# Optimization experiments

Hardware: AMD Instinct MI355X
Metric: run time of the kernel (lower is better)

## Reference

```python
import jax, jax.numpy as jnp
import numpy as np

D = 1024
H = 16
HD = D // H
MLP = 4 * D


def _lin(key, fin, fout):
    k1, k2 = jax.random.split(key)
    lim = 1.0 / np.sqrt(fin)
    W = jax.random.uniform(k1, (fin, fout), minval=-lim, maxval=lim, dtype=jnp.float32)
    b = jax.random.uniform(k2, (fout,), minval=-lim, maxval=lim, dtype=jnp.float32)
    return W, b


def setup_inputs() -> dict:
    key = jax.random.key(0)
    ks = jax.random.split(key, 10)
    x = jax.random.normal(ks[0], (4, 2048, D), dtype=jnp.float32)
    time_emb = jax.random.normal(ks[1], (4, D), dtype=jnp.float32)
    Wqkv, bqkv = _lin(ks[2], D, 3 * D)
    Wproj, bproj = _lin(ks[3], D, D)
    W1, b1 = _lin(ks[4], D, MLP)
    W2, b2 = _lin(ks[5], MLP, D)
    Wt, bt = _lin(ks[6], D, 6 * D)
    g1 = jnp.ones((D,), jnp.float32); be1 = jnp.zeros((D,), jnp.float32)
    g2 = jnp.ones((D,), jnp.float32); be2 = jnp.zeros((D,), jnp.float32)
    return {"x": x, "time_emb": time_emb, "Wqkv": Wqkv, "bqkv": bqkv,
            "Wproj": Wproj, "bproj": bproj, "W1": W1, "b1": b1, "W2": W2, "b2": b2,
            "Wt": Wt, "bt": bt, "g1": g1, "be1": be1, "g2": g2, "be2": be2}


def layernorm(x, g, b, eps=1e-5):
    mu = jnp.mean(x, axis=-1, keepdims=True)
    var = jnp.var(x, axis=-1, keepdims=True)
    return (x - mu) * jax.lax.rsqrt(var + eps) * g + b


def attention(h, Wqkv, bqkv, Wproj, bproj):
    B, L, _ = h.shape
    qkv = (h @ Wqkv + bqkv).reshape(B, L, 3, H, HD)
    q, k, v = jnp.moveaxis(qkv, 2, 0)  # each [B,L,H,HD]
    scale = HD ** -0.5
    attn = jnp.einsum('blhd,bmhd->bhlm', q, k) * scale
    attn = jax.nn.softmax(attn, axis=-1)
    out = jnp.einsum('bhlm,bmhd->blhd', attn, v).reshape(B, L, D)
    return out @ Wproj + bproj


def reference(x, time_emb, Wqkv, bqkv, Wproj, bproj, W1, b1, W2, b2, Wt, bt, g1, be1, g2, be2):
    tp = (jax.nn.silu(time_emb) @ Wt + bt)[:, None, :]  # [B,1,6D]
    shift_msa, scale_msa, gate_msa, shift_mlp, scale_mlp, gate_mlp = jnp.split(tp, 6, axis=-1)
    h = layernorm(x, g1, be1)
    h = h * (1.0 + scale_msa) + shift_msa
    h = attention(h, Wqkv, bqkv, Wproj, bproj)
    x = x + gate_msa * h
    h = layernorm(x, g2, be2)
    h = h * (1.0 + scale_mlp) + shift_mlp
    h = jax.nn.gelu(h @ W1 + b1, approximate=False) @ W2 + b2
    x = x + gate_mlp * h
    return x
```

## Files before the change

### kernel.cpp

```cpp
#include <hip/hip_runtime.h>
#include <hip/hip_bf16.h>
#include <math.h>


typedef __attribute__((ext_vector_type(8))) __bf16 bf16x8;
typedef __attribute__((ext_vector_type(4))) float f32x4;

union FragU { uint4 u; bf16x8 b; };

#define AS1(p) ((const __attribute__((address_space(1))) void*)(p))
#define AS3(p) ((__attribute__((address_space(3))) void*)(p))

__device__ __forceinline__ float bflo(uint u) {
    union { uint i; float f; } v; v.i = u << 16; return v.f;
}
__device__ __forceinline__ float bfhi(uint u) {
    union { uint i; float f; } v; v.i = u & 0xffff0000u; return v.f;
}
__device__ __forceinline__ ushort f2bf(float f) {
    union { float f; uint i; } v; v.f = f;
    uint r = (v.i + 0x7fffu + ((v.i >> 16) & 1u)) >> 16;
    return (ushort)r;
}
__device__ __forceinline__ uint pkbf(float a, float b) {
    return __builtin_amdgcn_perm(__float_as_uint(b), __float_as_uint(a), 0x07060302u);
}
__device__ __forceinline__ void stval(ushort* p, float v) { *p = f2bf(v); }
__device__ __forceinline__ void stval(float* p, float v) { *p = v; }

__device__ __forceinline__ float gelu_f(float x) {
    float y = 0.7978845608f * (x + 0.044715f * x * x * x);
    float e = exp2f(y * 2.88539008178f);
    float t = 1.f - 2.f / (1.f + e);
    return 0.5f * x * (1.f + t);
}

__global__ __launch_bounds__(256) void transpose_f2b(const float* __restrict__ in,
                                                     ushort* __restrict__ out,
                                                     int R, int C) {
    __shared__ ushort t[32][33];
    int c0 = blockIdx.x * 32, r0 = blockIdx.y * 32;
    int tx = threadIdx.x, ty = threadIdx.y;
#pragma unroll
    for (int i = 0; i < 32; i += 8)
        t[ty + i][tx] = f2bf(in[(size_t)(r0 + ty + i) * C + c0 + tx]);
    __syncthreads();
#pragma unroll
    for (int i = 0; i < 32; i += 8)
        out[(size_t)(c0 + ty + i) * R + r0 + tx] = t[tx][ty + i];
}

__global__ __launch_bounds__(256) void transpose_v(const ushort* __restrict__ qkv,
                                                   ushort* __restrict__ vT) {
    int bh = blockIdx.x >> 5, lt = blockIdx.x & 31;
    int b = bh >> 4, h = bh & 15;
    int d = threadIdx.x & 63, lg = threadIdx.x >> 6;
    const ushort* src = qkv + (size_t)b * 2048 * 3072 + 2048 + h * 64 + d;
#pragma unroll
    for (int g = 0; g < 2; g++) {
        int l0 = lt * 64 + lg * 16 + g * 8;
        ushort v[8];
#pragma unroll
        for (int i = 0; i < 8; i++) v[i] = src[(size_t)(l0 + i) * 3072];
        *(uint4*)&vT[((size_t)bh * 64 + d) * 2048 + l0] = *(uint4*)v;
    }
}

__global__ __launch_bounds__(256) void tp_gemm(const float* __restrict__ te,
                                               const ushort* __restrict__ WtT,
                                               const float* __restrict__ bt,
                                               float* __restrict__ tp) {
    int w = blockIdx.x * 4 + (threadIdx.x >> 6);
    int lane = threadIdx.x & 63;
    int b = w / 6144, n = w % 6144;
    const ushort* wr = WtT + (size_t)n * 1024;
    const float* tr = te + (size_t)b * 1024;
    float s = 0.f;
#pragma unroll
    for (int i = 0; i < 16; i++) {
        int k = lane + 64 * i;
        float t = tr[k];
        float sil = t / (1.f + __expf(-t));
        s += sil * bflo((uint)wr[k]);
    }
#pragma unroll
    for (int x = 32; x; x >>= 1) s += __shfl_xor(s, x);
    if (lane == 0) tp[(size_t)b * 6144 + n] = s + bt[n];
}

__global__ __launch_bounds__(256) void ln_mod(const float* __restrict__ x,
                                              const float* __restrict__ tpb,
                                              const float* __restrict__ g,
                                              const float* __restrict__ be,
                                              ushort* __restrict__ out,
                                              int shift_off, int scale_off) {
    __shared__ float2 sred[4];
    int row = blockIdx.x;
    int b = row >> 11;
    int tid = threadIdx.x;
    float4 f = *(const float4*)&x[(size_t)row * 1024 + tid * 4];
    float v[4] = {f.x, f.y, f.z, f.w};
    float s = v[0] + v[1] + v[2] + v[3];
    float s2 = v[0] * v[0] + v[1] * v[1] + v[2] * v[2] + v[3] * v[3];
#pragma unroll
    for (int m = 32; m; m >>= 1) { s += __shfl_xor(s, m); s2 += __shfl_xor(s2, m); }
    if ((tid & 63) == 0) sred[tid >> 6] = make_float2(s, s2);
    __syncthreads();
    s = sred[0].x + sred[1].x + sred[2].x + sred[3].x;
    s2 = sred[0].y + sred[1].y + sred[2].y + sred[3].y;
    float mu = s * (1.f / 1024.f);
    float var = s2 * (1.f / 1024.f) - mu * mu;
    float rs = rsqrtf(var + 1e-5f);
    const float* tprow = tpb + (size_t)b * 6144;
    ushort o4[4];
#pragma unroll
    for (int t = 0; t < 4; t++) {
        int c = tid * 4 + t;
        float y = (v[t] - mu) * rs * g[c] + be[c];
        y = y * (1.f + tprow[scale_off + c]) + tprow[shift_off + c];
        o4[t] = f2bf(y);
    }
    *(uint2*)&out[(size_t)row * 1024 + tid * 4] = *(uint2*)o4;
}

template <int EPI, typename OT>
__global__ __launch_bounds__(256) void gemm_bt(const ushort* __restrict__ A,
                                               const ushort* __restrict__ BT,
                                               const float* __restrict__ bias,
                                               OT* __restrict__ C,
                                               int M, int N, int K,
                                               const float* __restrict__ res,
                                               const float* __restrict__ tpb,
                                               int goff) {
    __shared__ __align__(16) ushort As[2][128 * 32];
    __shared__ __align__(16) ushort Bs[2][128 * 32];
    int m0 = blockIdx.y * 128, n0 = blockIdx.x * 128;
    int tid = threadIdx.x;
    int wid = tid >> 6, lane = tid & 63;
    int wy = wid >> 1, wx = wid & 1;
    int r16 = lane & 15;
    int q8 = (lane >> 4) << 3;

    f32x4 acc[4][4];
#pragma unroll
    for (int i = 0; i < 4; i++)
#pragma unroll
        for (int j = 0; j < 4; j++) acc[i][j] = (f32x4){0.f, 0.f, 0.f, 0.f};

    int sr = tid >> 2;
    int sc = (tid & 3) << 3;
    const ushort* Abase = A + (size_t)(m0 + sr) * K + sc;
    const ushort* Bbase = BT + (size_t)(n0 + sr) * K + sc;

    for (int k0 = 0; k0 < K; k0 += 64) {
#pragma unroll
        for (int c = 0; c < 2; c++) {
            ushort* AsW = As[c] + wid * 512;
            ushort* BsW = Bs[c] + wid * 512;
            int kk = k0 + 32 * c;
            __builtin_amdgcn_global_load_lds(AS1(Abase + kk), AS3(AsW), 16, 0, 0);
            __builtin_amdgcn_global_load_lds(AS1(Abase + (size_t)64 * K + kk), AS3(AsW + 2048), 16, 0, 0);
            __builtin_amdgcn_global_load_lds(AS1(Bbase + kk), AS3(BsW), 16, 0, 0);
            __builtin_amdgcn_global_load_lds(AS1(Bbase + (size_t)64 * K + kk), AS3(BsW + 2048), 16, 0, 0);
        }
        __syncthreads();
#pragma unroll
        for (int c = 0; c < 2; c++) {
            FragU fa[4], fb[4];
#pragma unroll
            for (int i = 0; i < 4; i++)
                fa[i].u = *(const uint4*)&As[c][(wy * 64 + i * 16 + r16) * 32 + q8];
#pragma unroll
            for (int j = 0; j < 4; j++)
                fb[j].u = *(const uint4*)&Bs[c][(wx * 64 + j * 16 + r16) * 32 + q8];
#pragma unroll
            for (int i = 0; i < 4; i++)
#pragma unroll
                for (int j = 0; j < 4; j++)
                    acc[i][j] = __builtin_amdgcn_mfma_f32_16x16x32_bf16(fa[i].b, fb[j].b, acc[i][j], 0, 0, 0);
        }
        __syncthreads();
    }

    int q4 = (lane >> 4) << 2;
#pragma unroll
    for (int i = 0; i < 4; i++) {
#pragma unroll
        for (int j = 0; j < 4; j++) {
            int col = n0 + wx * 64 + j * 16 + r16;
            float bv = bias[col];
#pragma unroll
            for (int t = 0; t < 4; t++) {
                int row = m0 + wy * 64 + i * 16 + q4 + t;
                float v = acc[i][j][t] + bv;
                if constexpr (EPI == 1) {
                    v = gelu_f(v);
                }
                if constexpr (EPI == 2) {
                    float rv = res[(size_t)row * N + col];
                    float gate = tpb[(size_t)(row >> 11) * 6144 + goff + col];
                    v = rv + gate * v;
                }
                stval(&C[(size_t)row * N + col], v);
            }
        }
    }
}

__global__ __launch_bounds__(256, 5) void attn_mfma(const ushort* __restrict__ qkv,
                                                    const ushort* __restrict__ vT,
                                                    ushort* __restrict__ out) {
    __shared__ __align__(16) ushort Ks[64 * 72];
    __shared__ __align__(16) ushort Vs[64 * 72];
    __shared__ __align__(16) ushort Ps[64 * 72];

    int tid = threadIdx.x;
    int wid = tid >> 6, lane = tid & 63;
    int r16 = lane & 15, quad = lane >> 4;
    int q8 = quad << 3, q4 = quad << 2;

    int bh = blockIdx.x >> 5;
    int qt = blockIdx.x & 31;
    int b = bh >> 4, h = bh & 15;
    const ushort* qkbase = qkv + (size_t)b * 2048 * 3072 + h * 64;
    const float SC = 0.18033688011f;

    {
        int r = tid >> 2;
        int c = (tid & 3) << 4;
        const ushort* qp = qkbase + (size_t)(qt * 64 + r) * 3072 + c;
        *(uint4*)&Ps[r * 72 + c] = *(const uint4*)qp;
        *(uint4*)&Ps[r * 72 + c + 8] = *(const uint4*)(qp + 8);
    }
    __syncthreads();
    FragU qa[2];
#pragma unroll
    for (int ks = 0; ks < 2; ks++)
        qa[ks].u = *(const uint4*)&Ps[(wid * 16 + r16) * 72 + ks * 32 + q8];

    float l_ = 0.f;
    f32x4 o[4];
#pragma unroll
    for (int dn = 0; dn < 4; dn++) o[dn] = (f32x4){0.f, 0.f, 0.f, 0.f};

    int kr = tid >> 2;
    int kc = (tid & 3) << 4;
    const ushort* kptr = qkbase + 1024 + (size_t)kr * 3072 + kc;
    const ushort* vptr = vT + (size_t)bh * 131072 + (size_t)kr * 2048 + kc;

    uint4 ka0 = *(const uint4*)kptr;
    uint4 ka1 = *(const uint4*)(kptr + 8);
    uint4 va0 = *(const uint4*)vptr;
    uint4 va1 = *(const uint4*)(vptr + 8);

    for (int kt = 0; kt < 32; kt++) {
        __syncthreads();
        *(uint4*)&Ks[kr * 72 + kc] = ka0;
        *(uint4*)&Ks[kr * 72 + kc + 8] = ka1;
        *(uint4*)&Vs[kr * 72 + kc] = va0;
        *(uint4*)&Vs[kr * 72 + kc + 8] = va1;
        __syncthreads();

        if (kt < 31) {
            const ushort* kp2 = kptr + (size_t)(kt + 1) * 64 * 3072;
            const ushort* vp2 = vptr + (kt + 1) * 64;
            ka0 = *(const uint4*)kp2;
            ka1 = *(const uint4*)(kp2 + 8);
            va0 = *(const uint4*)vp2;
            va1 = *(const uint4*)(vp2 + 8);
        }

        f32x4 s[4];
#pragma unroll
        for (int n = 0; n < 4; n++) s[n] = (f32x4){0.f, 0.f, 0.f, 0.f};
#pragma unroll
        for (int ks = 0; ks < 2; ks++) {
            FragU kb[4];
#pragma unroll
            for (int n = 0; n < 4; n++)
                kb[n].u = *(const uint4*)&Ks[(n * 16 + r16) * 72 + ks * 32 + q8];
#pragma unroll
            for (int n = 0; n < 4; n++)
                s[n] = __builtin_amdgcn_mfma_f32_16x16x32_bf16(kb[n].b, qa[ks].b, s[n], 0, 0, 0);
        }

        float p[4][4];
#pragma unroll
        for (int n = 0; n < 4; n++)
#pragma unroll
            for (int t = 0; t < 4; t++) {
                float a = fminf(s[n][t] * SC, 60.f);
                float pv = exp2f(a);
                p[n][t] = pv;
                l_ += pv;
            }

#pragma unroll
        for (int n = 0; n < 4; n++) {
            uint2 w2 = make_uint2(pkbf(p[n][0], p[n][1]), pkbf(p[n][2], p[n][3]));
            *(uint2*)&Ps[(wid * 16 + r16) * 72 + n * 16 + q4] = w2;
        }

#pragma unroll
        for (int ks = 0; ks < 2; ks++) {
            FragU pa, vb[4];
            pa.u = *(const uint4*)&Ps[(wid * 16 + r16) * 72 + ks * 32 + q8];
#pragma unroll
            for (int dn = 0; dn < 4; dn++)
                vb[dn].u = *(const uint4*)&Vs[(dn * 16 + r16) * 72 + ks * 32 + q8];
#pragma unroll
            for (int dn = 0; dn < 4; dn++)
                o[dn] = __builtin_amdgcn_mfma_f32_16x16x32_bf16(vb[dn].b, pa.b, o[dn], 0, 0, 0);
        }
    }

    l_ += __shfl_xor(l_, 16);
    l_ += __shfl_xor(l_, 32);
    float inv = 1.f / l_;
    int row = qt * 64 + wid * 16 + r16;
    ushort* orow = out + (size_t)(b * 2048 + row) * 1024 + h * 64;
#pragma unroll
    for (int dn = 0; dn < 4; dn++) {
        uint2 w2 = make_uint2(pkbf(o[dn][0] * inv, o[dn][1] * inv),
                              pkbf(o[dn][2] * inv, o[dn][3] * inv));
        *(uint2*)&orow[dn * 16 + q4] = w2;
    }
}

extern "C" void kernel_launch(void* const* d_in, const int* in_sizes, int n_in,
                              void* d_out, int out_size, void* d_ws, size_t ws_size,
                              hipStream_t stream) {
    const float* x    = (const float*)d_in[0];
    const float* te   = (const float*)d_in[1];
    const float* Wqkv = (const float*)d_in[2];
    const float* bqkv = (const float*)d_in[3];
    const float* Wproj= (const float*)d_in[4];
    const float* bproj= (const float*)d_in[5];
    const float* W1   = (const float*)d_in[6];
    const float* b1   = (const float*)d_in[7];
    const float* W2   = (const float*)d_in[8];
    const float* b2   = (const float*)d_in[9];
    const float* Wt   = (const float*)d_in[10];
    const float* bt   = (const float*)d_in[11];
    const float* g1   = (const float*)d_in[12];
    const float* be1  = (const float*)d_in[13];
    const float* g2   = (const float*)d_in[14];
    const float* be2  = (const float*)d_in[15];

    char* ws = (char*)d_ws;
    ushort* WqkvT  = (ushort*)(ws + 0);
    ushort* WprojT = (ushort*)(ws + 6291456);
    ushort* W1T    = (ushort*)(ws + 8388608);
    ushort* W2T    = (ushort*)(ws + 16777216);
    ushort* WtT    = (ushort*)(ws + 25165824);
    float*  tpb    = (float*)(ws + 37748736);
    ushort* hbuf   = (ushort*)(ws + 37847040);
    ushort* vTb    = (ushort*)(ws + 37847040);
    ushort* qkvb   = (ushort*)(ws + 54624256);
    ushort* midb   = (ushort*)(ws + 54624256);
    ushort* attnb  = (ushort*)(ws + 121733120);
    float*  x1b    = (float*)(ws + 138510336);

    dim3 tb(32, 8);
    hipLaunchKernelGGL(transpose_f2b, dim3(3072 / 32, 1024 / 32), tb, 0, stream, Wqkv, WqkvT, 1024, 3072);
    hipLaunchKernelGGL(transpose_f2b, dim3(1024 / 32, 1024 / 32), tb, 0, stream, Wproj, WprojT, 1024, 1024);
    hipLaunchKernelGGL(transpose_f2b, dim3(4096 / 32, 1024 / 32), tb, 0, stream, W1, W1T, 1024, 4096);
    hipLaunchKernelGGL(transpose_f2b, dim3(1024 / 32, 4096 / 32), tb, 0, stream, W2, W2T, 4096, 1024);
    hipLaunchKernelGGL(transpose_f2b, dim3(6144 / 32, 1024 / 32), tb, 0, stream, Wt, WtT, 1024, 6144);

    hipLaunchKernelGGL(tp_gemm, dim3(6144), dim3(256), 0, stream, te, WtT, bt, tpb);

    hipLaunchKernelGGL(ln_mod, dim3(8192), dim3(256), 0, stream, x, tpb, g1, be1, hbuf, 0, 1024);

    hipLaunchKernelGGL((gemm_bt<0, ushort>), dim3(3072 / 128, 8192 / 128), dim3(256), 0, stream,
                       hbuf, WqkvT, bqkv, qkvb, 8192, 3072, 1024, (const float*)nullptr, (const float*)nullptr, 0);

    hipLaunchKernelGGL(transpose_v, dim3(2048), dim3(256), 0, stream, qkvb, vTb);

    hipLaunchKernelGGL(attn_mfma, dim3(2048), dim3(256), 0, stream, qkvb, vTb, attnb);

    hipLaunchKernelGGL((gemm_bt<2, float>), dim3(1024 / 128, 8192 / 128), dim3(256), 0, stream,
                       attnb, WprojT, bproj, x1b, 8192, 1024, 1024, x, tpb, 2048);

    hipLaunchKernelGGL(ln_mod, dim3(8192), dim3(256), 0, stream, x1b, tpb, g2, be2, hbuf, 3072, 4096);

    hipLaunchKernelGGL((gemm_bt<1, ushort>), dim3(4096 / 128, 8192 / 128), dim3(256), 0, stream,
                       hbuf, W1T, b1, midb, 8192, 4096, 1024, (const float*)nullptr, (const float*)nullptr, 0);

    hipLaunchKernelGGL((gemm_bt<2, float>), dim3(1024 / 128, 8192 / 128), dim3(256), 0, stream,
                       midb, W2T, b2, (float*)d_out, 8192, 1024, 4096, x1b, tpb, 5120);
}
```

Before: 631.9 us.

## Enlarge attention query tile to 128 rows and fold softmax scale into QKV GEMM

The attention kernel now uses 512 threads (8 waves) per block, each block covering 128 query rows, so every K/V tile loaded into shared memory serves twice as many queries. Each thread now loads one 16-byte chunk of K and of V per tile instead of two. The softmax scale (with log2e) is multiplied into the Q columns in the QKV GEMM epilogue, which removes a per-element multiply from the attention inner loop. The row-sum is split into four partial accumulators to shorten the dependency chain. The costs are higher register and LDS pressure per block under launch_bounds(512,8), and Q is now rounded to bf16 after scaling.

Result: slower. 678.8 us (+7.4%).

```diff
diff --git a/kernel.cpp b/kernel.cpp
--- a/kernel.cpp
+++ b/kernel.cpp
@@ -13,9 +13,6 @@
 
 __device__ __forceinline__ float bflo(uint u) {
     union { uint i; float f; } v; v.i = u << 16; return v.f;
-}
-__device__ __forceinline__ float bfhi(uint u) {
-    union { uint i; float f; } v; v.i = u & 0xffff0000u; return v.f;
 }
 __device__ __forceinline__ ushort f2bf(float f) {
     union { float f; uint i; } v; v.f = f;
@@ -131,7 +128,7 @@
                                                int M, int N, int K,
                                                const float* __restrict__ res,
                                                const float* __restrict__ tpb,
-                                               int goff) {
+                                               int goff, int sccols) {
     __shared__ __align__(16) ushort As[2][128 * 32];
     __shared__ __align__(16) ushort Bs[2][128 * 32];
     int m0 = blockIdx.y * 128, n0 = blockIdx.x * 128;
@@ -193,6 +190,9 @@
             for (int t = 0; t < 4; t++) {
                 int row = m0 + wy * 64 + i * 16 + q4 + t;
                 float v = acc[i][j][t] + bv;
+                if constexpr (EPI == 0) {
+                    if (col < sccols) v *= 0.18033688011f;
+                }
                 if constexpr (EPI == 1) {
                     v = gelu_f(v);
                 }
@@ -207,28 +207,27 @@
     }
 }
 
-__global__ __launch_bounds__(256, 5) void attn_mfma(const ushort* __restrict__ qkv,
+__global__ __launch_bounds__(512, 8) void attn_mfma(const ushort* __restrict__ qkv,
                                                     const ushort* __restrict__ vT,
                                                     ushort* __restrict__ out) {
     __shared__ __align__(16) ushort Ks[64 * 72];
     __shared__ __align__(16) ushort Vs[64 * 72];
-    __shared__ __align__(16) ushort Ps[64 * 72];
+    __shared__ __align__(16) ushort Ps[128 * 72];
 
     int tid = threadIdx.x;
     int wid = tid >> 6, lane = tid & 63;
     int r16 = lane & 15, quad = lane >> 4;
     int q8 = quad << 3, q4 = quad << 2;
 
-    int bh = blockIdx.x >> 5;
-    int qt = blockIdx.x & 31;
+    int bh = blockIdx.x >> 4;
+    int qt = blockIdx.x & 15;
     int b = bh >> 4, h = bh & 15;
     const ushort* qkbase = qkv + (size_t)b * 2048 * 3072 + h * 64;
-    const float SC = 0.18033688011f;
 
     {
         int r = tid >> 2;
         int c = (tid & 3) << 4;
-        const ushort* qp = qkbase + (size_t)(qt * 64 + r) * 3072 + c;
+        const ushort* qp = qkbase + (size_t)(qt * 128 + r) * 3072 + c;
         *(uint4*)&Ps[r * 72 + c] = *(const uint4*)qp;
         *(uint4*)&Ps[r * 72 + c + 8] = *(const uint4*)(qp + 8);
     }
@@ -238,36 +237,28 @@
     for (int ks = 0; ks < 2; ks++)
         qa[ks].u = *(const uint4*)&Ps[(wid * 16 + r16) * 72 + ks * 32 + q8];
 
-    float l_ = 0.f;
+    float l4[4] = {0.f, 0.f, 0.f, 0.f};
     f32x4 o[4];
 #pragma unroll
     for (int dn = 0; dn < 4; dn++) o[dn] = (f32x4){0.f, 0.f, 0.f, 0.f};
 
-    int kr = tid >> 2;
-    int kc = (tid & 3) << 4;
+    int kr = tid >> 3;
+    int kc = (tid & 7) << 3;
     const ushort* kptr = qkbase + 1024 + (size_t)kr * 3072 + kc;
     const ushort* vptr = vT + (size_t)bh * 131072 + (size_t)kr * 2048 + kc;
 
-    uint4 ka0 = *(const uint4*)kptr;
-    uint4 ka1 = *(const uint4*)(kptr + 8);
-    uint4 va0 = *(const uint4*)vptr;
-    uint4 va1 = *(const uint4*)(vptr + 8);
+    uint4 ka = *(const uint4*)kptr;
+    uint4 va = *(const uint4*)vptr;
 
     for (int kt = 0; kt < 32; kt++) {
         __syncthreads();
-        *(uint4*)&Ks[kr * 72 + kc] = ka0;
-        *(uint4*)&Ks[kr * 72 + kc + 8] = ka1;
-        *(uint4*)&Vs[kr * 72 + kc] = va0;
-        *(uint4*)&Vs[kr * 72 + kc + 8] = va1;
+        *(uint4*)&Ks[kr * 72 + kc] = ka;
+        *(uint4*)&Vs[kr * 72 + kc] = va;
         __syncthreads();
 
         if (kt < 31) {
-            const ushort* kp2 = kptr + (size_t)(kt + 1) * 64 * 3072;
-            const ushort* vp2 = vptr + (kt + 1) * 64;
-            ka0 = *(const uint4*)kp2;
-            ka1 = *(const uint4*)(kp2 + 8);
-            va0 = *(const uint4*)vp2;
-            va1 = *(const uint4*)(vp2 + 8);
+            ka = *(const uint4*)(kptr + (size_t)(kt + 1) * 64 * 3072);
+            va = *(const uint4*)(vptr + (kt + 1) * 64);
         }
 
         f32x4 s[4];
@@ -289,10 +280,9 @@
         for (int n = 0; n < 4; n++)
 #pragma unroll
             for (int t = 0; t < 4; t++) {
-                float a = fminf(s[n][t] * SC, 60.f);
-                float pv = exp2f(a);
+                float pv = exp2f(fminf(s[n][t], 60.f));
                 p[n][t] = pv;
-                l_ += pv;
+                l4[t] += pv;
             }
 
 #pragma unroll
@@ -314,10 +304,11 @@
         }
     }
 
+    float l_ = (l4[0] + l4[1]) + (l4[2] + l4[3]);
     l_ += __shfl_xor(l_, 16);
     l_ += __shfl_xor(l_, 32);
     float inv = 1.f / l_;
-    int row = qt * 64 + wid * 16 + r16;
+    int row = qt * 128 + wid * 16 + r16;
     ushort* orow = out + (size_t)(b * 2048 + row) * 1024 + h * 64;
 #pragma unroll
     for (int dn = 0; dn < 4; dn++) {
@@ -373,20 +364,20 @@
     hipLaunchKernelGGL(ln_mod, dim3(8192), dim3(256), 0, stream, x, tpb, g1, be1, hbuf, 0, 1024);
 
     hipLaunchKernelGGL((gemm_bt<0, ushort>), dim3(3072 / 128, 8192 / 128), dim3(256), 0, stream,
-                       hbuf, WqkvT, bqkv, qkvb, 8192, 3072, 1024, (const float*)nullptr, (const float*)nullptr, 0);
+                       hbuf, WqkvT, bqkv, qkvb, 8192, 3072, 1024, (const float*)nullptr, (const float*)nullptr, 0, 1024);
 
     hipLaunchKernelGGL(transpose_v, dim3(2048), dim3(256), 0, stream, qkvb, vTb);
 
-    hipLaunchKernelGGL(attn_mfma, dim3(2048), dim3(256), 0, stream, qkvb, vTb, attnb);
+    hipLaunchKernelGGL(attn_mfma, dim3(1024), dim3(512), 0, stream, qkvb, vTb, attnb);
 
     hipLaunchKernelGGL((gemm_bt<2, float>), dim3(1024 / 128, 8192 / 128), dim3(256), 0, stream,
-                       attnb, WprojT, bproj, x1b, 8192, 1024, 1024, x, tpb, 2048);
+                       attnb, WprojT, bproj, x1b, 8192, 1024, 1024, x, tpb, 2048, 0);
 
     hipLaunchKernelGGL(ln_mod, dim3(8192), dim3(256), 0, stream, x1b, tpb, g2, be2, hbuf, 3072, 4096);
 
     hipLaunchKernelGGL((gemm_bt<1, ushort>), dim3(4096 / 128, 8192 / 128), dim3(256), 0, stream,
-                       hbuf, W1T, b1, midb, 8192, 4096, 1024, (const float*)nullptr, (const float*)nullptr, 0);
+                       hbuf, W1T, b1, midb, 8192, 4096, 1024, (const float*)nullptr, (const float*)nullptr, 0, 0);
 
     hipLaunchKernelGGL((gemm_bt<2, float>), dim3(1024 / 128, 8192 / 128), dim3(256), 0, stream,
-                       midb, W2T, b2, (float*)d_out, 8192, 1024, 4096, x1b, tpb, 5120);
-}
+                       midb, W2T, b2, (float*)d_out, 8192, 1024, 4096, x1b, tpb, 5120, 0);
+}
```
